# Kernel optimization log

Measured on AMD Instinct MI355X. Metric: run time of the kernel, lower is better.

Reference implementation:

```python
import jax, jax.numpy as jnp
import numpy as np

PATCH = 3  # patch_size

def _extract_patches(feat):
    # feat: (c, h, w) -> (n_patches, c*9), patches in row-major spatial order
    c, h, w = feat.shape
    p = jax.lax.conv_general_dilated_patches(feat[None], (PATCH, PATCH), (1, 1), 'VALID')
    return p[0].reshape(c * PATCH * PATCH, -1).T  # (n, c*9)

def _match_single(feat_in, feat_ref):
    # faithful to feature_match_index(is_norm=True, norm_input=True)
    c, h, w = feat_in.shape
    def pxnorm(f):
        # F.normalize over channel dim per pixel (eps=1e-12)
        v = f.reshape(c, -1)
        n = jnp.sqrt(jnp.sum(v * v, axis=0, keepdims=True))
        return (v / jnp.maximum(n, 1e-12)).reshape(c, h, w)
    fi = pxnorm(feat_in)
    fr = pxnorm(feat_ref)
    pin = _extract_patches(fi)    # (n_in, c*9)
    pref = _extract_patches(fr)   # (n_ref, c*9)
    pref = pref / (jnp.sqrt(jnp.sum(pref * pref, axis=1, keepdims=True)) + 1e-5)
    corr = pin @ pref.T           # (n_in, n_ref) dense correlation volume
    max_idx = jnp.argmax(corr, axis=1)
    max_val = jnp.max(corr, axis=1)
    max_val = max_val / (jnp.sqrt(jnp.sum(pin * pin, axis=1)) + 1e-5)  # norm_input
    hh, ww = h - PATCH + 1, w - PATCH + 1
    return max_idx.reshape(hh, ww), max_val.reshape(hh, ww)

def _index_to_flow(max_idx):
    # max_idx: (B, hh, ww) int -> flow (B, hh+2, ww+2, 2), channels = (dx, dy)
    B, hh, ww = max_idx.shape
    fw = (max_idx % ww).astype(jnp.float32)
    fh = (max_idx // ww).astype(jnp.float32)
    gx = jnp.arange(ww, dtype=jnp.float32)[None, None, :]
    gy = jnp.arange(hh, dtype=jnp.float32)[None, :, None]
    flow = jnp.stack([fw - gx, fh - gy], axis=-1)
    return jnp.pad(flow, ((0, 0), (0, 2), (0, 2), (0, 0)))

def _shift(x, sh, sw):
    # tensor_shift with fill 0: new[:, sh:, sw:] = x[:, :h-sh, :w-sw]
    B, h, w, c = x.shape
    return jnp.pad(x, ((0, 0), (sh, 0), (sw, 0), (0, 0)))[:, :h, :w, :]

def _conv(x, w, b):
    y = jax.lax.conv_general_dilated(x, w, (1, 1), 'SAME',
                                     dimension_numbers=('NCHW', 'OIHW', 'NCHW'))
    return y + b[None, :, None, None]

def _pool(x):
    return jax.lax.reduce_window(x, -jnp.inf, jax.lax.max, (1, 1, 2, 2), (1, 1, 2, 2), 'VALID')

def _vgg(img, w11, b11, w12, b12, w21, b21, w22, b22, w31, b31):
    mean = jnp.array([0.485, 0.456, 0.406], jnp.float32).reshape(1, 3, 1, 1)
    std = jnp.array([0.229, 0.224, 0.225], jnp.float32).reshape(1, 3, 1, 1)
    x = (img - mean) / std
    x = jax.nn.relu(_conv(x, w11, b11)); relu1_1 = x
    x = jax.nn.relu(_conv(x, w12, b12))
    x = _pool(x)
    x = jax.nn.relu(_conv(x, w21, b21)); relu2_1 = x
    x = jax.nn.relu(_conv(x, w22, b22))
    x = _pool(x)
    x = jax.nn.relu(_conv(x, w31, b31)); relu3_1 = x
    return relu1_1, relu2_1, relu3_1

def setup_inputs() -> dict:
    key = jax.random.key(0)
    ks = jax.random.split(key, 8)
    B, C, H, W = 4, 256, 64, 64
    inp = {}
    inp['dense_features1'] = jax.random.normal(ks[0], (B, C, H, W), jnp.float32)
    inp['dense_features2'] = jax.random.normal(ks[1], (B, C, H, W), jnp.float32)
    inp['img_ref_hr'] = jax.random.uniform(ks[2], (B, 3, 4 * H, 4 * W), dtype=jnp.float32)
    def cw(k, o, i):
        return jax.random.normal(k, (o, i, 3, 3), jnp.float32) * np.sqrt(2.0 / (i * 9))
    inp['w11'] = cw(ks[3], 64, 3);    inp['b11'] = jnp.zeros((64,), jnp.float32)
    inp['w12'] = cw(ks[4], 64, 64);   inp['b12'] = jnp.zeros((64,), jnp.float32)
    inp['w21'] = cw(ks[5], 128, 64);  inp['b21'] = jnp.zeros((128,), jnp.float32)
    inp['w22'] = cw(ks[6], 128, 128); inp['b22'] = jnp.zeros((128,), jnp.float32)
    inp['w31'] = cw(ks[7], 256, 128); inp['b31'] = jnp.zeros((256,), jnp.float32)
    return inp

def reference(dense_features1, dense_features2, img_ref_hr,
              w11, b11, w12, b12, w21, b21, w22, b22, w31, b31):
    max_idx, max_val = jax.vmap(_match_single)(dense_features1, dense_features2)
    # relu3 scale
    sim3 = jnp.pad(max_val, ((0, 0), (1, 1), (1, 1)))[:, None]        # (B,1,h,w)
    flow3 = _index_to_flow(max_idx)                                    # (B,h,w,2)
    off3 = jnp.stack([_shift(flow3, i, j) for i in range(3) for j in range(3)], axis=1)
    # relu2 scale (x2)
    sim2 = jnp.repeat(jnp.repeat(sim3, 2, axis=2), 2, axis=3)
    flow2 = jnp.repeat(jnp.repeat(flow3, 2, axis=1), 2, axis=2) * 2.0
    off2 = jnp.stack([_shift(flow2, 2 * i, 2 * j) for i in range(3) for j in range(3)], axis=1)
    # relu1 scale (x4)
    sim1 = jnp.repeat(jnp.repeat(sim2, 2, axis=2), 2, axis=3)
    flow1 = jnp.repeat(jnp.repeat(flow3, 4, axis=1), 4, axis=2) * 4.0
    off1 = jnp.stack([_shift(flow1, 4 * i, 4 * j) for i in range(3) for j in range(3)], axis=1)
    relu1_1, relu2_1, relu3_1 = _vgg(img_ref_hr, w11, b11, w12, b12, w21, b21, w22, b22, w31, b31)
    return (off3, off2, off1, flow3, flow2, flow1, sim3, sim2, sim1, relu1_1, relu2_1, relu3_1)
```

## Files before the change

### kernel.cpp

```cpp
#include <hip/hip_runtime.h>
#include <cstdint>
#include <cstddef>

#define HW 4096
#define NPQ 3844

typedef __attribute__((ext_vector_type(8))) short bf16x8;
typedef __attribute__((ext_vector_type(4))) float f32x4;
typedef unsigned short ushort;
typedef unsigned int uint;

__device__ __forceinline__ ushort f2bu(float f){
  uint u = __float_as_uint(f);
  uint r = (u + 0x7fffu + ((u >> 16) & 1u)) >> 16;
  return (ushort)r;
}
__device__ __forceinline__ uint umax2x16(uint a, uint b){
  uint ah = a >> 16, bh = b >> 16, al = a & 0xffffu, bl = b & 0xffffu;
  uint h = ah > bh ? ah : bh, l = al > bl ? al : bl;
  return (h << 16) | l;
}


__global__ __launch_bounds__(256) void k_norm2(const float* __restrict__ fA,
                                               const float* __restrict__ fB,
                                               float* __restrict__ fnA,
                                               float* __restrict__ fnB,
                                               float* __restrict__ spixA,
                                               float* __restrict__ spixB,
                                               size_t inStride, size_t outStride,
                                               int sStride){
  const size_t zb = blockIdx.z;
  const float* f  = (blockIdx.y ? fB  : fA) + zb*inStride;
  float* fn       = (blockIdx.y ? fnB : fnA) + zb*outStride;
  float* spix     = (blockIdx.y ? spixB : spixA) + zb*(size_t)sStride;
  __shared__ float red[16][17];
  const int px = threadIdx.x & 15, cg = threadIdx.x >> 4;
  const int pix = blockIdx.x*16 + px;
  float s = 0.f;
  #pragma unroll
  for (int i=0;i<16;i++){ float v = f[(cg*16+i)*HW + pix]; s += v*v; }
  red[cg][px] = s; __syncthreads();
  for (int off=8; off>0; off>>=1){
    if (cg < off) red[cg][px] += red[cg+off][px];
    __syncthreads();
  }
  float n = fmaxf(sqrtf(red[0][px]), 1e-12f);
  float s2 = 0.f;
  #pragma unroll
  for (int i=0;i<16;i++){
    float v = f[(cg*16+i)*HW + pix] / n;
    fn[(cg*16+i)*HW + pix] = v;
    s2 += v*v;
  }
  __syncthreads();
  red[cg][px] = s2; __syncthreads();
  for (int off=8; off>0; off>>=1){
    if (cg < off) red[cg][px] += red[cg+off][px];
    __syncthreads();
  }
  if (cg == 0) spix[pix] = red[0][px];
}

__global__ __launch_bounds__(256) void k_normpq(const float* __restrict__ s1,
                                                const float* __restrict__ s2,
                                                float* __restrict__ normP,
                                                float* __restrict__ normQ,
                                                int sStride, int nStride){
  int p = blockIdx.x*256 + threadIdx.x;
  if (p >= NPQ) return;
  const size_t zb = blockIdx.z;
  s1 += zb*(size_t)sStride; s2 += zb*(size_t)sStride;
  normP += zb*(size_t)nStride; normQ += zb*(size_t)nStride;
  int py = p/62, px = p - py*62;
  float a=0.f, b=0.f;
  for (int dy=0;dy<3;dy++)
    for (int dx=0;dx<3;dx++){
      int o = (py+dy)*64 + px+dx;
      a += s1[o]; b += s2[o];
    }
  normP[p] = sqrtf(a) + 1e-5f;
  normQ[p] = sqrtf(b) + 1e-5f;
}

__global__ __launch_bounds__(256) void k_gemm(const float* __restrict__ A,
                                              const float* __restrict__ B,
                                              float* __restrict__ E,
                                              size_t abStride, size_t eStride){
  __shared__ float As[16][128];
  __shared__ float Bs[16][256];
  const size_t zb = blockIdx.z;
  A += zb*abStride; B += zb*abStride; E += zb*eStride;
  const int m0 = blockIdx.y*128, n0 = blockIdx.x*256;
  const int tid = threadIdx.x;
  const int ty = tid>>4, tx = tid&15;

  const int arow = tid>>5;
  const int acol = (tid&31)*4;
  const int brow = tid>>6;
  const int bcol = (tid&63)*4;

  const float* Ag = A + (size_t)arow*HW + m0 + acol;
  const float* Bg = B + (size_t)brow*HW + n0 + bcol;

  float4 pa0 = *(const float4*)(Ag);
  float4 pa1 = *(const float4*)(Ag + (size_t)8*HW);
  float4 pb0 = *(const float4*)(Bg);
  float4 pb1 = *(const float4*)(Bg + (size_t)4*HW);
  float4 pb2 = *(const float4*)(Bg + (size_t)8*HW);
  float4 pb3 = *(const float4*)(Bg + (size_t)12*HW);

  float acc[8][16];
  #pragma unroll
  for (int i=0;i<8;i++)
    #pragma unroll
    for (int j=0;j<16;j++) acc[i][j]=0.f;

  for (int t=0;t<16;t++){
    __syncthreads();
    *(float4*)&As[arow][acol]    = pa0;
    *(float4*)&As[arow+8][acol]  = pa1;
    *(float4*)&Bs[brow][bcol]    = pb0;
    *(float4*)&Bs[brow+4][bcol]  = pb1;
    *(float4*)&Bs[brow+8][bcol]  = pb2;
    *(float4*)&Bs[brow+12][bcol] = pb3;
    __syncthreads();
    if (t < 15){
      const float* An = Ag + (size_t)(t+1)*16*HW;
      const float* Bn = Bg + (size_t)(t+1)*16*HW;
      pa0 = *(const float4*)(An);
      pa1 = *(const float4*)(An + (size_t)8*HW);
      pb0 = *(const float4*)(Bn);
      pb1 = *(const float4*)(Bn + (size_t)4*HW);
      pb2 = *(const float4*)(Bn + (size_t)8*HW);
      pb3 = *(const float4*)(Bn + (size_t)12*HW);
    }
    #pragma unroll
    for (int k=0;k<16;k++){
      float4 a0 = *(const float4*)&As[k][ty*8];
      float4 a1 = *(const float4*)&As[k][ty*8+4];
      float4 b0 = *(const float4*)&Bs[k][tx*4];
      float4 b1 = *(const float4*)&Bs[k][64+tx*4];
      float4 b2 = *(const float4*)&Bs[k][128+tx*4];
      float4 b3 = *(const float4*)&Bs[k][192+tx*4];
      float a[8] = {a0.x,a0.y,a0.z,a0.w,a1.x,a1.y,a1.z,a1.w};
      float b[16] = {b0.x,b0.y,b0.z,b0.w,b1.x,b1.y,b1.z,b1.w,
                     b2.x,b2.y,b2.z,b2.w,b3.x,b3.y,b3.z,b3.w};
      #pragma unroll
      for (int i=0;i<8;i++)
        #pragma unroll
        for (int j=0;j<16;j++) acc[i][j] = fmaf(a[i], b[j], acc[i][j]);
    }
  }
  #pragma unroll
  for (int i=0;i<8;i++){
    float* rowp = E + (size_t)(m0+ty*8+i)*HW + n0;
    *(float4*)(rowp + tx*4)       = make_float4(acc[i][0], acc[i][1], acc[i][2], acc[i][3]);
    *(float4*)(rowp + 64 + tx*4)  = make_float4(acc[i][4], acc[i][5], acc[i][6], acc[i][7]);
    *(float4*)(rowp + 128 + tx*4) = make_float4(acc[i][8], acc[i][9], acc[i][10], acc[i][11]);
    *(float4*)(rowp + 192 + tx*4) = make_float4(acc[i][12], acc[i][13], acc[i][14], acc[i][15]);
  }
}

__global__ __launch_bounds__(256) void k_reduce(const float* __restrict__ E,
                                                const float* __restrict__ normP,
                                                const float* __restrict__ normQ,
                                                float* __restrict__ maxval,
                                                int* __restrict__ maxidx,
                                                size_t eStride, int nStride){
  const int p = blockIdx.x;
  const int bz = blockIdx.y;
  E += (size_t)bz*eStride;
  normP += (size_t)bz*(size_t)nStride;
  normQ += (size_t)bz*(size_t)nStride;
  const int py = p/62, px = p - py*62;
  const int t = threadIdx.x;
  float best = -3.0e38f; int bq = 1<<30;

  if (t < 248){
    const int qy = t >> 2, g = t & 3;
    const int qx0 = g*16;
    const int cnt = (g==3) ? 14 : 16;
    float s[16];
    #pragma unroll
    for (int j=0;j<16;j++) s[j]=0.f;
    #pragma unroll
    for (int dy=0;dy<3;dy++){
      const int cbase = (qy+dy)*64 + qx0;
      #pragma unroll
      for (int dx=0;dx<3;dx++){
        const float* row = E + (size_t)((py+dy)*64 + px+dx)*HW + cbase;
        float4 w0 = *(const float4*)(row);
        float4 w1 = *(const float4*)(row+4);
        float4 w2 = *(const float4*)(row+8);
        float4 w3 = *(const float4*)(row+12);
        float4 w4 = (g<3) ? *(const float4*)(row+16) : make_float4(0.f,0.f,0.f,0.f);
        float w[20] = {w0.x,w0.y,w0.z,w0.w, w1.x,w1.y,w1.z,w1.w,
                       w2.x,w2.y,w2.z,w2.w, w3.x,w3.y,w3.z,w3.w,
                       w4.x,w4.y,w4.z,w4.w};
        #pragma unroll
        for (int j=0;j<16;j++) s[j] += w[dx+j];
      }
    }
    const int qbase = qy*62 + qx0;
    for (int j=0;j<cnt;j++){
      float v = s[j] / normQ[qbase + j];
      if (v > best){ best = v; bq = qbase + j; }
    }
  }

  __shared__ float sv[256];
  __shared__ int si[256];
  sv[t] = best; si[t] = bq;
  __syncthreads();
  for (int off=128; off>0; off>>=1){
    if (t < off){
      float ov = sv[t+off]; int oi = si[t+off];
      float cv = sv[t];     int ci = si[t];
      if (ov > cv || (ov == cv && oi < ci)){ sv[t]=ov; si[t]=oi; }
    }
    __syncthreads();
  }
  if (t == 0){
    maxval[bz*NPQ + p] = sv[0] / normP[p];
    maxidx[bz*NPQ + p] = si[0];
  }
}


__global__ __launch_bounds__(256) void k_flow3(const int* __restrict__ maxidx,
                                               const float* __restrict__ maxval,
                                               float* __restrict__ flow3ws,
                                               float* __restrict__ sim3ws,
                                               float* __restrict__ oflow,
                                               float* __restrict__ osim){
  int idx = blockIdx.x*256 + threadIdx.x;
  if (idx >= 4*HW) return;
  int b = idx >> 12, r = idx & 4095;
  int y = r >> 6, x = r & 63;
  float fx = 0.f, fy = 0.f;
  if (y < 62 && x < 62){
    int mi = maxidx[b*NPQ + y*62 + x];
    int qy = mi/62, qx = mi - qy*62;
    fx = (float)(qx - x);
    fy = (float)(qy - y);
  }
  flow3ws[idx*2] = fx; flow3ws[idx*2+1] = fy;
  oflow[idx*2] = fx; oflow[idx*2+1] = fy;
  float sv = 0.f;
  if (y >= 1 && y <= 62 && x >= 1 && x <= 62)
    sv = maxval[b*NPQ + (y-1)*62 + (x-1)];
  sim3ws[idx] = sv;
  osim[idx] = sv;
}

__global__ __launch_bounds__(256) void k_off3(const float* __restrict__ flow3ws,
                                              float* __restrict__ out){
  int idx = blockIdx.x*256 + threadIdx.x;
  if (idx >= 4*9*HW) return;
  int b = idx / (9*HW);
  int rem = idx - b*9*HW;
  int k = rem >> 12;
  int r = rem & 4095;
  int y = r >> 6, x = r & 63;
  int i = k/3, j = k - i*3;
  float fx = 0.f, fy = 0.f;
  if (y >= i && x >= j){
    int s = (b*HW + (y-i)*64 + (x-j))*2;
    fx = flow3ws[s]; fy = flow3ws[s+1];
  }
  out[idx*2] = fx; out[idx*2+1] = fy;
}

__global__ __launch_bounds__(256) void k_flowS(const float* __restrict__ flow3ws,
                                               const float* __restrict__ sim3ws,
                                               float* __restrict__ oflow,
                                               float* __restrict__ osim,
                                               int S, int N){
  int idx = blockIdx.x*256 + threadIdx.x;
  int tot = 4*N*N;
  if (idx >= tot) return;
  int b = idx/(N*N);
  int r = idx - b*N*N;
  int y = r/N, x = r - y*N;
  int s = b*HW + (y/S)*64 + (x/S);
  float fx = flow3ws[s*2] * (float)S;
  float fy = flow3ws[s*2+1] * (float)S;
  oflow[idx*2] = fx; oflow[idx*2+1] = fy;
  osim[idx] = sim3ws[s];
}

__global__ __launch_bounds__(256) void k_offS(const float* __restrict__ flow3ws,
                                              float* __restrict__ out,
                                              int S, int N){
  int idx = blockIdx.x*256 + threadIdx.x;
  int tot = 4*9*N*N;
  if (idx >= tot) return;
  int b = idx/(9*N*N);
  int rem = idx - b*9*N*N;
  int k = rem/(N*N);
  int r = rem - k*(N*N);
  int y = r/N, x = r - y*N;
  int i = k/3, j = k - i*3;
  float fx = 0.f, fy = 0.f;
  int sy = y - S*i, sx = x - S*j;
  if (sy >= 0 && sx >= 0){
    int s = (b*HW + (sy/S)*64 + (sx/S))*2;
    fx = flow3ws[s] * (float)S;
    fy = flow3ws[s+1] * (float)S;
  }
  out[idx*2] = fx; out[idx*2+1] = fy;
}


__global__ __launch_bounds__(256) void k_wt(const float* __restrict__ w,
                                            ushort* __restrict__ wt,
                                            int Cout, int Cin){
  int idx = blockIdx.x*256 + threadIdx.x;
  int tot = Cout*Cin*9;
  if (idx >= tot) return;
  int o = idx / (Cin*9);
  int rem = idx - o*(Cin*9);
  int i = rem / 9;
  int tap = rem - i*9;
  wt[((size_t)tap*Cout + o)*Cin + i] = f2bu(w[idx]);
}

__global__ __launch_bounds__(256) void k_conv1(const float* __restrict__ img,
                                               const float* __restrict__ w,
                                               const float* __restrict__ bias,
                                               float* __restrict__ outf,
                                               ushort* __restrict__ outb){
  __shared__ float sIn[3][18][20];
  __shared__ float sW[8][3][9];
  const int tx = threadIdx.x & 15, ty = threadIdx.x >> 4;
  const int x0 = blockIdx.x*16, y0 = blockIdx.y*16;
  const int b = blockIdx.z >> 3;
  const int oc0 = (blockIdx.z & 7)*8;
  const float MEAN[3] = {0.485f,0.456f,0.406f};
  const float STDV[3] = {0.229f,0.224f,0.225f};
  const float* in = img + (size_t)b*3*65536;
  for (int i = threadIdx.x; i < 3*324; i += 256){
    int ci = i / 324;
    int rr = i - ci*324;
    int iy = rr / 18, ix = rr - iy*18;
    int gy = y0 + iy - 1, gx = x0 + ix - 1;
    float v = 0.f;
    if (gy >= 0 && gy < 256 && gx >= 0 && gx < 256)
      v = (in[ci*65536 + gy*256 + gx] - MEAN[ci]) / STDV[ci];
    sIn[ci][iy][ix] = v;
  }
  if (threadIdx.x < 216){
    int o = threadIdx.x / 27;
    int rr = threadIdx.x - o*27;
    int ci = rr / 9, t = rr - ci*9;
    sW[o][ci][t] = w[((oc0+o)*3 + ci)*9 + t];
  }
  __syncthreads();
  float acc[8] = {0.f,0.f,0.f,0.f,0.f,0.f,0.f,0.f};
  for (int ci=0; ci<3; ci++){
    #pragma unroll
    for (int ky=0;ky<3;ky++){
      #pragma unroll
      for (int kx=0;kx<3;kx++){
        float v = sIn[ci][ty+ky][tx+kx];
        #pragma unroll
        for (int o=0;o<8;o++)
          acc[o] = fmaf(v, sW[o][ci][ky*3+kx], acc[o]);
      }
    }
  }
  #pragma unroll
  for (int o=0;o<8;o++){
    float r = fmaxf(acc[o] + bias[oc0+o], 0.f);
    outf[(size_t)b*4194304 + (size_t)(oc0+o)*65536 + (size_t)(y0+ty)*256 + (x0+tx)] = r;
    outb[(size_t)b*4194304 + ((size_t)(y0+ty)*256 + (x0+tx))*64 + (oc0+o)] = f2bu(r);
  }
}

__global__ __launch_bounds__(256) void k_conv_mfma(const ushort* __restrict__ X,
                                                   const ushort* __restrict__ Wt,
                                                   const float* __restrict__ bias,
                                                   ushort* __restrict__ outHWC,
                                                   float* __restrict__ outCHW,
                                                   int Cin, int Cout, int H, int W,
                                                   int zDiv, size_t xStride,
                                                   size_t hwcStride, size_t chwStride){
  extern __shared__ ushort smem[];
  const int CS = Cin + 8;
  ushort* sX = smem;
  ushort* sW = smem + 10*18*CS;
  const int tid = threadIdx.x;
  const int wave = tid >> 6, lane = tid & 63;
  const int quad = lane >> 4, l16 = lane & 15;
  const int bz = blockIdx.z / zDiv;
  const int zo = blockIdx.z - bz*zDiv;
  const int x0 = blockIdx.x * 16, y0 = blockIdx.y * 8, oc0 = zo * 64;
  X += (size_t)bz * xStride;
  if (outHWC) outHWC += (size_t)bz * hwcStride;
  if (outCHW) outCHW += (size_t)bz * chwStride;
  const int nci8 = Cin >> 3;
  const int c8s = (Cin == 128) ? 4 : 3;
  const int c8m = nci8 - 1;

  for (int i = tid; i < 180*nci8; i += 256){
    int c8 = i & c8m;
    int rest = i >> c8s;
    int px = rest % 18;
    int row = rest / 18;
    int gy = y0 - 1 + row, gx = x0 - 1 + px;
    uint4 v = make_uint4(0u,0u,0u,0u);
    if (gy >= 0 && gy < H && gx >= 0 && gx < W)
      v = *(const uint4*)(X + ((size_t)gy*W + gx)*Cin + c8*8);
    *(uint4*)(sX + (row*18 + px)*CS + c8*8) = v;
  }

  f32x4 acc[2][4];
  #pragma unroll
  for (int m=0;m<2;m++)
    #pragma unroll
    for (int r=0;r<4;r++) acc[m][r] = (f32x4){0.f,0.f,0.f,0.f};

  const int my = (wave>>1)*4;
  const int mo = (wave&1)*32;

  for (int tap = 0; tap < 9; tap++){
    int dy = tap/3 - 1, dx = tap - (tap/3)*3 - 1;
    __syncthreads();
    const ushort* wsrc = Wt + ((size_t)tap*Cout + oc0)*Cin;
    for (int i = tid; i < 64*nci8; i += 256){
      int c8 = i & c8m, o = i >> c8s;
      *(uint4*)(sW + o*CS + c8*8) = *(const uint4*)(wsrc + o*Cin + c8*8);
    }
    __syncthreads();
    for (int k0 = 0; k0 < Cin; k0 += 32){
      bf16x8 A0 = *(const bf16x8*)(sW + (mo + l16)*CS + k0 + quad*8);
      bf16x8 A1 = *(const bf16x8*)(sW + (mo + 16 + l16)*CS + k0 + quad*8);
      #pragma unroll
      for (int r = 0; r < 4; r++){
        bf16x8 B = *(const bf16x8*)(sX + ((1 + my + r + dy)*18 + (1 + l16 + dx))*CS + k0 + quad*8);
        acc[0][r] = __builtin_amdgcn_mfma_f32_16x16x32_bf16(A0, B, acc[0][r], 0, 0, 0);
        acc[1][r] = __builtin_amdgcn_mfma_f32_16x16x32_bf16(A1, B, acc[1][r], 0, 0, 0);
      }
    }
  }

  const int x = x0 + l16;
  #pragma unroll
  for (int m = 0; m < 2; m++){
    int ocb = oc0 + mo + m*16 + quad*4;
    float4 bv = *(const float4*)(bias + ocb);
    #pragma unroll
    for (int r = 0; r < 4; r++){
      int y = y0 + my + r;
      float v0 = fmaxf(acc[m][r][0] + bv.x, 0.f);
      float v1 = fmaxf(acc[m][r][1] + bv.y, 0.f);
      float v2 = fmaxf(acc[m][r][2] + bv.z, 0.f);
      float v3 = fmaxf(acc[m][r][3] + bv.w, 0.f);
      if (outHWC){
        uint lo = (uint)f2bu(v0) | ((uint)f2bu(v1) << 16);
        uint hi = (uint)f2bu(v2) | ((uint)f2bu(v3) << 16);
        uint2* dst = (uint2*)(outHWC + ((size_t)y*W + x)*Cout + ocb);
        *dst = make_uint2(lo, hi);
      }
      if (outCHW){
        size_t base = (size_t)ocb*H*W + (size_t)y*W + x;
        outCHW[base]                 = v0;
        outCHW[base +   (size_t)H*W] = v1;
        outCHW[base + 2*(size_t)H*W] = v2;
        outCHW[base + 3*(size_t)H*W] = v3;
      }
    }
  }
}

__global__ __launch_bounds__(256) void k_pool_h(const ushort* __restrict__ in,
                                                ushort* __restrict__ out,
                                                int C, int Wo, int s,
                                                size_t inStride, size_t outStride){
  in  += (size_t)blockIdx.z * inStride;
  out += (size_t)blockIdx.z * outStride;
  int idx = blockIdx.x*256 + threadIdx.x;
  int nc8 = C >> 3;
  if (idx >= Wo*nc8) return;
  int x = idx >> s;
  int c8 = idx & (nc8 - 1);
  int y = blockIdx.y;
  int Wi = 2*Wo;
  const ushort* p = in + ((size_t)(2*y)*Wi + 2*x)*C + c8*8;
  uint4 a = *(const uint4*)p;
  uint4 b = *(const uint4*)(p + C);
  uint4 c = *(const uint4*)(p + (size_t)Wi*C);
  uint4 d = *(const uint4*)(p + (size_t)Wi*C + C);
  uint4 m;
  m.x = umax2x16(umax2x16(a.x,b.x), umax2x16(c.x,d.x));
  m.y = umax2x16(umax2x16(a.y,b.y), umax2x16(c.y,d.y));
  m.z = umax2x16(umax2x16(a.z,b.z), umax2x16(c.z,d.z));
  m.w = umax2x16(umax2x16(a.w,b.w), umax2x16(c.w,d.w));
  *(uint4*)(out + ((size_t)y*Wo + x)*C + c8*8) = m;
}


extern "C" void kernel_launch(void* const* d_in, const int* in_sizes, int n_in,
                              void* d_out, int out_size, void* d_ws, size_t ws_size,
                              hipStream_t stream){
  const float* f1  = (const float*)d_in[0];
  const float* f2  = (const float*)d_in[1];
  const float* img = (const float*)d_in[2];
  const float* w11 = (const float*)d_in[3];  const float* b11 = (const float*)d_in[4];
  const float* w12 = (const float*)d_in[5];  const float* b12 = (const float*)d_in[6];
  const float* w21 = (const float*)d_in[7];  const float* b21 = (const float*)d_in[8];
  const float* w22 = (const float*)d_in[9];  const float* b22 = (const float*)d_in[10];
  const float* w31 = (const float*)d_in[11]; const float* b31 = (const float*)d_in[12];
  float* out = (float*)d_out;

  float* F = (float*)d_ws;
  float* E = F;

  ushort* wt1  = (ushort*)(F + 16777216);
  ushort* wt2a = (ushort*)(F + 16795648);
  ushort* wt2b = (ushort*)(F + 16832512);
  ushort* wt3  = (ushort*)(F + 16906240);

  ushort* EU  = (ushort*)E;
  ushort* t1a = EU;
  ushort* t2a = EU + 16777216;
  ushort* p1a = EU;
  ushort* t3a = EU + 4194304;
  ushort* t4a = EU + 16777216;
  ushort* p2a = EU;

  const size_t O_OFF3 = 0, O_OFF2 = 294912, O_OFF1 = 1474560;
  const size_t O_FLOW3 = 6193152, O_FLOW2 = 6225920, O_FLOW1 = 6356992;
  const size_t O_SIM3 = 6881280, O_SIM2 = 6897664, O_SIM1 = 6963200;
  const size_t O_R1 = 7225344, O_R2 = 24002560, O_R3 = 32391168;

  const bool big = ws_size >= 302600000ull;

  float *mval, *fl3, *sm3; int* midx;

  if (big){
    float* f1n = F + 67108864;
    float* f2n = F + 71303168;
    float* s1  = F + 75497472;
    float* s2  = F + 75513856;
    float* nP  = F + 75530240;
    float* nQ  = F + 75546624;
    mval = F + 75563008;
    midx = (int*)(F + 75579392);
    fl3  = F + 75595776;
    sm3  = F + 75628544;

    k_norm2<<<dim3(256,2,4),256,0,stream>>>(f1, f2, f1n, f2n, s1, s2,
                                            (size_t)256*HW, 1048576, 4096);
    k_normpq<<<dim3(16,1,4),256,0,stream>>>(s1, s2, nP, nQ, 4096, 4096);
    k_gemm<<<dim3(16,32,4),256,0,stream>>>(f1n, f2n, E, 1048576, 16777216);
    k_reduce<<<dim3(NPQ,4),256,0,stream>>>(E, nP, nQ, mval, midx, 16777216, 4096);
  } else {
    float* f1n  = F + 16777216;
    float* f2n  = F + 17825792;
    float* s1   = F + 18874368;
    float* s2   = F + 18878464;
    float* nP   = F + 18882560;
    float* nQ   = F + 18886656;
    mval = F + 18890752;
    midx = (int*)(F + 18907136);
    fl3  = F + 18923520;
    sm3  = F + 18956288;

    for (int b=0;b<4;b++){
      const float* f1b  = f1 + (size_t)b*256*HW;
      const float* f2b2 = f2 + (size_t)b*256*HW;
      k_norm2<<<dim3(256,2,1),256,0,stream>>>(f1b, f2b2, f1n, f2n, s1, s2, 0, 0, 0);
      k_normpq<<<dim3(16,1,1),256,0,stream>>>(s1, s2, nP, nQ, 0, 0);
      k_gemm<<<dim3(16,32,1),256,0,stream>>>(f1n, f2n, E, 0, 0);
      k_reduce<<<dim3(NPQ,1),256,0,stream>>>(E, nP, nQ, mval + b*NPQ, midx + b*NPQ, 0, 0);
    }
  }

  k_flow3<<<64,256,0,stream>>>(midx, mval, fl3, sm3, out+O_FLOW3, out+O_SIM3);
  k_off3<<<576,256,0,stream>>>(fl3, out+O_OFF3);
  k_flowS<<<256,256,0,stream>>>(fl3, sm3, out+O_FLOW2, out+O_SIM2, 2, 128);
  k_offS<<<2304,256,0,stream>>>(fl3, out+O_OFF2, 2, 128);
  k_flowS<<<1024,256,0,stream>>>(fl3, sm3, out+O_FLOW1, out+O_SIM1, 4, 256);
  k_offS<<<9216,256,0,stream>>>(fl3, out+O_OFF1, 4, 256);

  k_wt<<<144,256,0,stream>>>(w12, wt1, 64, 64);
  k_wt<<<288,256,0,stream>>>(w21, wt2a, 128, 64);
  k_wt<<<576,256,0,stream>>>(w22, wt2b, 128, 128);
  k_wt<<<1152,256,0,stream>>>(w31, wt3, 256, 128);

  const int smem64  = (180*72  + 64*72)  * 2;
  const int smem128 = (180*136 + 64*136) * 2;

  k_conv1<<<dim3(16,16,32),256,0,stream>>>(img, w11, b11, out + O_R1, t1a);
  k_conv_mfma<<<dim3(16,32,4),256,smem64,stream>>>(t1a, wt1, b12, t2a, nullptr,
      64, 64, 256, 256, 1, 4194304, 4194304, 0);
  k_pool_h<<<dim3(4,128,4),256,0,stream>>>(t2a, p1a, 64, 128, 3, 4194304, 1048576);
  k_conv_mfma<<<dim3(8,16,8),256,smem64,stream>>>(p1a, wt2a, b21, t3a, out + O_R2,
      64, 128, 128, 128, 2, 1048576, 2097152, 2097152);
  k_conv_mfma<<<dim3(8,16,8),256,smem128,stream>>>(t3a, wt2b, b22, t4a, nullptr,
      128, 128, 128, 128, 2, 2097152, 2097152, 0);
  k_pool_h<<<dim3(4,64,4),256,0,stream>>>(t4a, p2a, 128, 64, 4, 2097152, 524288);
  k_conv_mfma<<<dim3(4,8,16),256,smem128,stream>>>(p2a, wt3, b31, nullptr, out + O_R3,
      128, 256, 64, 64, 4, 524288, 0, 1048576);
}
```

Before: 1.124 ms.

## Double-buffer GEMM tiles in LDS using direct global-to-LDS loads

The fp32 correlation GEMM now loads its A and B tiles straight into LDS with global_load_lds, into two alternating buffers. The next tile is fetched while the current one is being multiplied. This removes the register staging and one barrier per k-step. In exchange, LDS use doubles to 48KB per block, which may lower occupancy. Correctness also depends on the load having finished before the barrier.

```diff
diff --git a/kernel.cpp b/kernel.cpp
--- a/kernel.cpp
+++ b/kernel.cpp
@@ -19,6 +19,12 @@
   uint ah = a >> 16, bh = b >> 16, al = a & 0xffffu, bl = b & 0xffffu;
   uint h = ah > bh ? ah : bh, l = al > bl ? al : bl;
   return (h << 16) | l;
+}
+
+__device__ __forceinline__ void gll16(const float* g, float* l){
+  __builtin_amdgcn_global_load_lds(
+      (const __attribute__((address_space(1))) void*)g,
+      (__attribute__((address_space(3))) void*)l, 16, 0, 0);
 }
 
 
@@ -87,28 +93,21 @@
                                               const float* __restrict__ B,
                                               float* __restrict__ E,
                                               size_t abStride, size_t eStride){
-  __shared__ float As[16][128];
-  __shared__ float Bs[16][256];
+  __shared__ __align__(16) float As[2][16][128];
+  __shared__ __align__(16) float Bs[2][16][256];
   const size_t zb = blockIdx.z;
   A += zb*abStride; B += zb*abStride; E += zb*eStride;
   const int m0 = blockIdx.y*128, n0 = blockIdx.x*256;
   const int tid = threadIdx.x;
   const int ty = tid>>4, tx = tid&15;
+  const int wave = tid>>6;
 
   const int arow = tid>>5;
   const int acol = (tid&31)*4;
   const int brow = tid>>6;
   const int bcol = (tid&63)*4;
-
   const float* Ag = A + (size_t)arow*HW + m0 + acol;
   const float* Bg = B + (size_t)brow*HW + n0 + bcol;
-
-  float4 pa0 = *(const float4*)(Ag);
-  float4 pa1 = *(const float4*)(Ag + (size_t)8*HW);
-  float4 pb0 = *(const float4*)(Bg);
-  float4 pb1 = *(const float4*)(Bg + (size_t)4*HW);
-  float4 pb2 = *(const float4*)(Bg + (size_t)8*HW);
-  float4 pb3 = *(const float4*)(Bg + (size_t)12*HW);
 
   float acc[8][16];
   #pragma unroll
@@ -116,33 +115,40 @@
     #pragma unroll
     for (int j=0;j<16;j++) acc[i][j]=0.f;
 
+  {
+    float* ad = &As[0][0][0] + wave*256;
+    float* bd = &Bs[0][0][0] + wave*256;
+    gll16(Ag,                    ad);
+    gll16(Ag + (size_t)8*HW,     ad + 1024);
+    gll16(Bg,                    bd);
+    gll16(Bg + (size_t)4*HW,     bd + 1024);
+    gll16(Bg + (size_t)8*HW,     bd + 2048);
+    gll16(Bg + (size_t)12*HW,    bd + 3072);
+  }
+  __syncthreads();
+
   for (int t=0;t<16;t++){
-    __syncthreads();
-    *(float4*)&As[arow][acol]    = pa0;
-    *(float4*)&As[arow+8][acol]  = pa1;
-    *(float4*)&Bs[brow][bcol]    = pb0;
-    *(float4*)&Bs[brow+4][bcol]  = pb1;
-    *(float4*)&Bs[brow+8][bcol]  = pb2;
-    *(float4*)&Bs[brow+12][bcol] = pb3;
-    __syncthreads();
+    const int cur = t&1;
     if (t < 15){
       const float* An = Ag + (size_t)(t+1)*16*HW;
       const float* Bn = Bg + (size_t)(t+1)*16*HW;
-      pa0 = *(const float4*)(An);
-      pa1 = *(const float4*)(An + (size_t)8*HW);
-      pb0 = *(const float4*)(Bn);
-      pb1 = *(const float4*)(Bn + (size_t)4*HW);
-      pb2 = *(const float4*)(Bn + (size_t)8*HW);
-      pb3 = *(const float4*)(Bn + (size_t)12*HW);
+      float* ad = &As[cur^1][0][0] + wave*256;
+      float* bd = &Bs[cur^1][0][0] + wave*256;
+      gll16(An,                  ad);
+      gll16(An + (size_t)8*HW,   ad + 1024);
+      gll16(Bn,                  bd);
+      gll16(Bn + (size_t)4*HW,   bd + 1024);
+      gll16(Bn + (size_t)8*HW,   bd + 2048);
+      gll16(Bn + (size_t)12*HW,  bd + 3072);
     }
     #pragma unroll
     for (int k=0;k<16;k++){
-      float4 a0 = *(const float4*)&As[k][ty*8];
-      float4 a1 = *(const float4*)&As[k][ty*8+4];
-      float4 b0 = *(const float4*)&Bs[k][tx*4];
-      float4 b1 = *(const float4*)&Bs[k][64+tx*4];
-      float4 b2 = *(const float4*)&Bs[k][128+tx*4];
-      float4 b3 = *(const float4*)&Bs[k][192+tx*4];
+      float4 a0 = *(const float4*)&As[cur][k][ty*8];
+      float4 a1 = *(const float4*)&As[cur][k][ty*8+4];
+      float4 b0 = *(const float4*)&Bs[cur][k][tx*4];
+      float4 b1 = *(const float4*)&Bs[cur][k][64+tx*4];
+      float4 b2 = *(const float4*)&Bs[cur][k][128+tx*4];
+      float4 b3 = *(const float4*)&Bs[cur][k][192+tx*4];
       float a[8] = {a0.x,a0.y,a0.z,a0.w,a1.x,a1.y,a1.z,a1.w};
       float b[16] = {b0.x,b0.y,b0.z,b0.w,b1.x,b1.y,b1.z,b1.w,
                      b2.x,b2.y,b2.z,b2.w,b3.x,b3.y,b3.z,b3.w};
@@ -151,7 +157,9 @@
         #pragma unroll
         for (int j=0;j<16;j++) acc[i][j] = fmaf(a[i], b[j], acc[i][j]);
     }
-  }
+    __syncthreads();
+  }
+
   #pragma unroll
   for (int i=0;i<8;i++){
     float* rowp = E + (size_t)(m0+ty*8+i)*HW + n0;
```

Result: faster. 1.051 ms (-6.5%).
